# Kernel tuning notes

Measured on AMD Instinct MI355X. Metric: run time of the kernel, lower is better.

## Reference

```python
import jax, jax.numpy as jnp
import numpy as np

B, IN, U = 16, 1024, 1024


def _wSw(W, S):
    # W: [i,u], S: [b,i,i] -> W^T S W : [b,u,u]
    return jnp.einsum('iu,bij,jv->buv', W, S, W)


def _xSx(x, Wsig):
    # (sum_i x_i^2) * W_Sigma, broadcast over batch
    return jnp.sum(x * x, axis=1)[:, None, None] * Wsig


def _trS(S, Wsig):
    return jnp.trace(S, axis1=1, axis2=2)[:, None, None] * Wsig


def _hadamard_sigma(s1, s2, m1, m2):
    # s1*s2 + diag(m1) s2 diag(m1) + diag(m2) s1 diag(m2)
    return (s1 * s2
            + m1[:, :, None] * s2 * m1[:, None, :]
            + m2[:, :, None] * s1 * m2[:, None, :])


def _act_sigma(g, S):
    # S * outer(g, g)
    return S * (g[:, :, None] * g[:, None, :])


def setup_inputs() -> dict:
    key = jax.random.key(0)
    ks = jax.random.split(key, 16)
    f32 = jnp.float32
    init_mu, ini_sigma = 0.05, -4.6
    inp = {
        'mu_inputs': jax.random.normal(ks[0], (B, IN), f32),
        'sigma_inputs': 0.01 * jax.random.normal(ks[1], (B, IN, IN), f32),
        'prev_state': 0.1 * jax.random.normal(ks[2], (B, U), f32),
        'Sigma_state': 0.01 * jax.random.normal(ks[3], (B, U, U), f32),
        'U_z': init_mu * jax.random.normal(ks[4], (IN, U), f32),
        'uz_sigma': jnp.full((U,), ini_sigma, f32),
        'W_z': init_mu * jax.random.normal(ks[5], (U, U), f32),
        'wz_sigma': jnp.full((U,), ini_sigma, f32),
        'U_r': init_mu * jax.random.normal(ks[6], (IN, U), f32),
        'ur_sigma': jnp.full((U,), ini_sigma, f32),
        'W_r': init_mu * jax.random.normal(ks[7], (U, U), f32),
        'wr_sigma': jnp.full((U,), ini_sigma, f32),
        'U_h': init_mu * jax.random.normal(ks[8], (IN, U), f32),
        'uh_sigma': jnp.full((U,), ini_sigma, f32),
        'W_h': init_mu * jax.random.normal(ks[9], (U, U), f32),
        'wh_sigma': jnp.full((U,), ini_sigma, f32),
    }
    return inp


def reference(mu_inputs, sigma_inputs, prev_state, Sigma_state,
              U_z, uz_sigma, W_z, wz_sigma,
              U_r, ur_sigma, W_r, wr_sigma,
              U_h, uh_sigma, W_h, wh_sigma):
    sp = jax.nn.softplus
    # ---- z gate ----
    pre_z = mu_inputs @ U_z + prev_state @ W_z
    z = jax.nn.sigmoid(pre_z)
    Uz_S, Wz_S = jnp.diag(sp(uz_sigma)), jnp.diag(sp(wz_sigma))
    Sigma_zz = (_wSw(U_z, sigma_inputs) + _xSx(mu_inputs, Uz_S) + _trS(sigma_inputs, Uz_S)
                + _wSw(W_z, Sigma_state) + _xSx(prev_state, Wz_S) + _trS(Sigma_state, Wz_S))
    Sigma_z = _act_sigma(z * (1.0 - z), Sigma_zz)  # analytic d sigmoid
    # ---- r gate ----
    pre_r = mu_inputs @ U_r + prev_state @ W_r
    r = jax.nn.sigmoid(pre_r)
    Ur_S, Wr_S = jnp.diag(sp(ur_sigma)), jnp.diag(sp(wr_sigma))
    Sigma_rr = (_wSw(U_r, sigma_inputs) + _xSx(mu_inputs, Ur_S) + _trS(sigma_inputs, Ur_S)
                + _wSw(W_r, Sigma_state) + _xSx(prev_state, Wr_S) + _trS(Sigma_state, Wr_S))
    Sigma_r = _act_sigma(r * (1.0 - r), Sigma_rr)
    # ---- h gate ----
    sr = prev_state * r
    pre_h = mu_inputs @ U_h + sr @ W_h
    h = jnp.tanh(pre_h)
    Uh_S, Wh_S = jnp.diag(sp(uh_sigma)), jnp.diag(sp(wh_sigma))
    sigma_g = _hadamard_sigma(Sigma_state, Sigma_r, prev_state, r)
    Sigma_hh = (_wSw(U_h, sigma_inputs) + _xSx(mu_inputs, Uh_S) + _trS(sigma_inputs, Uh_S)
                + _wSw(W_h, sigma_g) + _xSx(sr, Wh_S) + _trS(sigma_g, Wh_S))
    Sigma_h = _act_sigma(1.0 - h * h, Sigma_hh)  # analytic d tanh
    # ---- combine ----
    mu_out = z * prev_state + (1.0 - z) * h
    sigma_a = _hadamard_sigma(Sigma_z, Sigma_state, z, prev_state)
    sigma_b = _hadamard_sigma(Sigma_z, Sigma_h, 1.0 - z, h)
    sigma_ab = Sigma_z * (prev_state[:, :, None] * h[:, None, :])
    sigma_abT = Sigma_z * (h[:, :, None] * prev_state[:, None, :])
    Sigma_out = sigma_a + sigma_b - sigma_ab - sigma_abT
    Sigma_out = jnp.where(jnp.isfinite(Sigma_out), Sigma_out, jnp.zeros_like(Sigma_out))
    eye = jnp.eye(Sigma_out.shape[-1], dtype=bool)
    Sigma_out = jnp.where(eye, jnp.abs(Sigma_out), Sigma_out)
    return mu_out, Sigma_out
```

## Files before the change

kernel.cpp:

```cpp
#include <hip/hip_runtime.h>
#include <math.h>


#define B_  16
#define N_  1024
#define NN_ (1024*1024)

typedef __bf16 bf16x8 __attribute__((ext_vector_type(8)));
typedef float  f32x4  __attribute__((ext_vector_type(4)));
typedef unsigned short ushort8v __attribute__((ext_vector_type(8)));

__device__ __forceinline__ unsigned short f2bf(float f) {
  union { float f; unsigned int u; } v; v.f = f;
  unsigned int r = v.u + 0x7fffu + ((v.u >> 16) & 1u);
  return (unsigned short)(r >> 16);
}
__device__ __forceinline__ float bf2f(unsigned short h) {
  union { unsigned int u; float f; } v; v.u = ((unsigned int)h) << 16;
  return v.f;
}

__device__ __forceinline__ void gload_lds16(const void* g, void* l) {
  __builtin_amdgcn_global_load_lds((__attribute__((address_space(1))) void*)g,
                                   (__attribute__((address_space(3))) void*)l,
                                   16, 0, 0);
}

#define MFMA_ __builtin_amdgcn_mfma_f32_16x16x32_bf16
#define SYNC_()  do { asm volatile("s_waitcnt lgkmcnt(0)" ::: "memory"); \
                      __builtin_amdgcn_sched_barrier(0); \
                      __builtin_amdgcn_s_barrier(); \
                      __builtin_amdgcn_sched_barrier(0); } while (0)

template<int OMODE, int PAIR>
__global__ __launch_bounds__(512)
void gemm8p(const unsigned short* __restrict__ A, int lda, long aStride, int koffA,
            const unsigned short* __restrict__ Bm, const unsigned short* __restrict__ Bm2,
            int ldb, long bStride, int K,
            void* __restrict__ Out, int ldo, long oStride, int noff,
            const float* __restrict__ act,
            const float* __restrict__ spU, const float* __restrict__ spW,
            const float* __restrict__ dU, const float* __restrict__ dW,
            const unsigned short* __restrict__ SzP, const float* __restrict__ SstP,
            const float* __restrict__ zV, const float* __restrict__ prevV,
            const float* __restrict__ hV)
{
  __shared__ __align__(16) char ldsb[163840];
  const int id = blockIdx.x;
  const int xcd = id & 7, rest = id >> 3;
  const int mt = rest & 3, pp = rest >> 2;
  const int panel = xcd + (pp << 3);
  const int nt = panel & 3;
  const int b  = (panel >> 2) & 15;
  const int ps = PAIR ? (panel >> 6) : 0;
  const unsigned short* Bsel = (PAIR && ps) ? Bm2 : Bm;
  const int kofx = koffA + (ps ? 1024 : 0);
  const int nofx = noff  + (ps ? 1024 : 0);
  const int mbase = mt << 8, nbase = nt << 8;
  const int tid = threadIdx.x, lane = tid & 63, w = tid >> 6;
  const int wm = w >> 2, wn = w & 3;
  const int NT = K >> 6;

  f32x4 acc[8][4];
  const f32x4 zero4 = {0.f, 0.f, 0.f, 0.f};
#pragma unroll
  for (int i = 0; i < 8; i++)
#pragma unroll
    for (int j = 0; j < 4; j++) acc[i][j] = zero4;

  const int l3 = lane >> 3, l7 = lane & 7;
  const int posg = l7 ^ l3;
  const int gr = (l3 << 1) + (posg >> 2);
  const int gc = (posg & 3) << 3;
  const int bi0 = w << 1, bi1 = bi0 + 1;
  const int rS0 = ((bi0 >> 1) << 4) + gr, cS0 = ((bi0 & 1) << 5) + gc;
  const int rS1 = ((bi1 >> 1) << 4) + gr, cS1 = ((bi1 & 1) << 5) + gc;
  const unsigned short* Ab = A + (size_t)b * aStride + (size_t)mbase * lda + kofx;
  const unsigned short* Bb = Bsel + (size_t)b * bStride + (size_t)nbase * ldb;
  const int d0 = w << 11, d1 = (w << 11) + 1024;

  auto SA = [&](int tt, int h) {
    char* dst = ldsb + ((tt & 1) << 15) + (h << 14);
    const unsigned short* s = Ab + (size_t)(h << 7) * lda + ((size_t)tt << 6);
    gload_lds16(s + (size_t)rS0 * lda + cS0, dst + d0);
    gload_lds16(s + (size_t)rS1 * lda + cS1, dst + d1);
  };
  auto SB = [&](int tt, int h) {
    char* dst = ldsb + 65536 + (tt % 3) * 32768 + (h << 14);
    const unsigned short* s = Bb + (size_t)(h << 7) * ldb + ((size_t)tt << 6);
    gload_lds16(s + (size_t)rS0 * ldb + cS0, dst + d0);
    gload_lds16(s + (size_t)rS1 * ldb + cS1, dst + d1);
  };

  const int lrow = lane & 15, c4 = lane >> 4;
  const int aoff = ((lrow >> 1) << 7) + (((((lrow & 1) << 2) | c4) ^ (lrow >> 1)) << 4);
  const int abase = wm << 14;
  const int bbase = ((wn >> 1) << 14);
  const int brg   = (wn & 1) << 2;
  auto LDA = [&](const char* pa, int mi, int ks) -> bf16x8 {
    return *(const bf16x8*)(pa + abase + (((mi << 1) + ks) << 10) + aoff);
  };
  auto LDB = [&](const char* pbv, int ni, int ks) -> bf16x8 {
    return *(const bf16x8*)(pbv + bbase + ((((brg + ni) << 1) + ks) << 10) + aoff);
  };

  SA(0, 0); SA(0, 1); SB(0, 0); SB(0, 1);
  if (NT > 1) { SB(1, 0); SB(1, 1); }
  asm volatile("s_waitcnt vmcnt(4)" ::: "memory");
  __builtin_amdgcn_sched_barrier(0);
  __builtin_amdgcn_s_barrier();
  __builtin_amdgcn_sched_barrier(0);

  bf16x8 avA[4], avB[4], bvA[4], bvB[4];
#pragma unroll
  for (int i = 0; i < 4; i++) avB[i] = LDA(ldsb, i, 0);
#pragma unroll
  for (int i = 0; i < 4; i++) bvB[i] = LDB(ldsb + 65536, i, 0);
  __builtin_amdgcn_sched_barrier(0);

  int bs = 0;
  for (int kt = 0; kt < NT; ++kt) {
    const char* pa = ldsb + ((kt & 1) << 15);
    const char* pbv = ldsb + 65536 + bs * 32768;
    const int bsn = (bs == 2) ? 0 : bs + 1;
    const char* pan = ldsb + (((kt + 1) & 1) << 15);
    const char* pbn = ldsb + 65536 + bsn * 32768;
#pragma unroll
    for (int i = 0; i < 4; i++) avA[i] = LDA(pa, 4 + i, 0);
    if (kt + 1 < NT) SA(kt + 1, 0);
    __builtin_amdgcn_s_setprio(1);
#pragma unroll
    for (int ni = 0; ni < 4; ni++)
#pragma unroll
      for (int mi = 0; mi < 4; mi++)
        acc[mi][ni] = MFMA_(avB[mi], bvB[ni], acc[mi][ni], 0, 0, 0);
    __builtin_amdgcn_s_setprio(0);
#pragma unroll
    for (int i = 0; i < 4; i++) avB[i] = LDA(pa, i, 1);
#pragma unroll
    for (int i = 0; i < 4; i++) bvA[i] = LDB(pbv, i, 1);
    if (kt + 1 < NT) SA(kt + 1, 1);
    __builtin_amdgcn_s_setprio(1);
#pragma unroll
    for (int ni = 0; ni < 4; ni++)
#pragma unroll
      for (int mi = 0; mi < 4; mi++)
        acc[4 + mi][ni] = MFMA_(avA[mi], bvB[ni], acc[4 + mi][ni], 0, 0, 0);
    __builtin_amdgcn_s_setprio(0);
#pragma unroll
    for (int i = 0; i < 4; i++) avA[i] = LDA(pa, 4 + i, 1);
    __builtin_amdgcn_s_setprio(1);
#pragma unroll
    for (int ni = 0; ni < 4; ni++)
#pragma unroll
      for (int mi = 0; mi < 4; mi++)
        acc[mi][ni] = MFMA_(avB[mi], bvA[ni], acc[mi][ni], 0, 0, 0);
    __builtin_amdgcn_s_setprio(0);
    if (kt + 2 < NT) {
      SB(kt + 2, 0); SB(kt + 2, 1);
      asm volatile("s_waitcnt vmcnt(4)" ::: "memory");
    } else {
      asm volatile("s_waitcnt vmcnt(0)" ::: "memory");
    }
    SYNC_();
    if (kt + 1 < NT) {
#pragma unroll
      for (int i = 0; i < 4; i++) avB[i] = LDA(pan, i, 0);
#pragma unroll
      for (int i = 0; i < 4; i++) bvB[i] = LDB(pbn, i, 0);
    }
    __builtin_amdgcn_sched_barrier(0);
    __builtin_amdgcn_s_setprio(1);
#pragma unroll
    for (int ni = 0; ni < 4; ni++)
#pragma unroll
      for (int mi = 0; mi < 4; mi++)
        acc[4 + mi][ni] = MFMA_(avA[mi], bvA[ni], acc[4 + mi][ni], 0, 0, 0);
    __builtin_amdgcn_s_setprio(0);
    bs = bsn;
  }

  __syncthreads();
  unsigned short* scr = (unsigned short*)(ldsb + w * 16384);
  const float* actb = act ? (act + b * N_) : nullptr;
  float dUb = 0.f, dWb = 0.f;
  if (OMODE != 0) { dUb = dU[b]; dWb = dW[b]; }

#pragma unroll
  for (int mi = 0; mi < 8; mi++) {
    const int rl0 = mi * 16 + ((lane >> 4) << 2);
#pragma unroll
    for (int ni = 0; ni < 4; ni++) {
      const int cl = ni * 16 + (lane & 15);
#pragma unroll
      for (int r = 0; r < 4; r++) {
        const int rl = rl0 + r;
        float val = acc[mi][ni][r];
        if (OMODE != 0) {
          const int u = mbase + wm * 128 + rl, v = nbase + wn * 64 + cl;
          if (u == v) val += dUb * spU[u] + dWb * spW[u];
          val *= actb[u] * actb[v];
        }
        scr[rl * 64 + ((((cl >> 3) ^ (rl & 7))) << 3) + (cl & 7)] = f2bf(val);
      }
    }
  }
  asm volatile("s_waitcnt lgkmcnt(0)" ::: "memory");
  __builtin_amdgcn_sched_barrier(0);

#pragma unroll
  for (int pq = 0; pq < 16; pq++) {
    const int row = pq * 8 + (lane >> 3);
    const int slot = lane & 7;
    const int ch = slot ^ (row & 7);
    const int u = mbase + wm * 128 + row;
    const int v0 = nbase + wn * 64 + (ch << 3);
    ushort8v s8 = *(const ushort8v*)&scr[row * 64 + (slot << 3)];
    if (OMODE == 0 || OMODE == 1) {
      unsigned short* ob = (unsigned short*)Out + (size_t)b * oStride
                         + (size_t)u * ldo + nofx + v0;
      *(ushort8v*)ob = s8;
    } else if (OMODE == 3) {
      const float pu = prevV[b * N_ + u];
      const float ru = zV[b * N_ + u];
      const ushort8v st8 = *(const ushort8v*)(SzP + (size_t)b * NN_ + (size_t)u * N_ + v0);
      const f32x4 pv0 = *(const f32x4*)(prevV + b * N_ + v0);
      const f32x4 pv1 = *(const f32x4*)(prevV + b * N_ + v0 + 4);
      const f32x4 rv0 = *(const f32x4*)(zV + b * N_ + v0);
      const f32x4 rv1 = *(const f32x4*)(zV + b * N_ + v0 + 4);
      ushort8v o8;
#pragma unroll
      for (int q = 0; q < 8; q++) {
        const float srv = bf2f((unsigned short)s8[q]);
        const float stt = bf2f((unsigned short)st8[q]);
        const float pv = (q < 4) ? pv0[q] : pv1[q - 4];
        const float rv = (q < 4) ? rv0[q] : rv1[q - 4];
        o8[q] = f2bf(stt * srv + pu * pv * srv + ru * rv * stt);
      }
      unsigned short* ob = (unsigned short*)Out + (size_t)b * oStride
                         + (size_t)u * ldo + v0;
      *(ushort8v*)ob = o8;
    } else {
      const float zu = zV[b * N_ + u];
      const float pu = prevV[b * N_ + u];
      const float hu = hV[b * N_ + u];
      const ushort8v sz8 = *(const ushort8v*)(SzP + (size_t)b * NN_ + (size_t)u * N_ + v0);
      const f32x4 st0 = *(const f32x4*)(SstP + (size_t)b * NN_ + (size_t)u * N_ + v0);
      const f32x4 st1 = *(const f32x4*)(SstP + (size_t)b * NN_ + (size_t)u * N_ + v0 + 4);
      const f32x4 zv0 = *(const f32x4*)(zV + b * N_ + v0);
      const f32x4 zv1 = *(const f32x4*)(zV + b * N_ + v0 + 4);
      const f32x4 pv0 = *(const f32x4*)(prevV + b * N_ + v0);
      const f32x4 pv1 = *(const f32x4*)(prevV + b * N_ + v0 + 4);
      const f32x4 hv0 = *(const f32x4*)(hV + b * N_ + v0);
      const f32x4 hv1 = *(const f32x4*)(hV + b * N_ + v0 + 4);
      f32x4 o0, o1;
#pragma unroll
      for (int q = 0; q < 8; q++) {
        const float shh = bf2f((unsigned short)s8[q]);
        const float szv = bf2f((unsigned short)sz8[q]);
        const float stt = (q < 4) ? st0[q] : st1[q - 4];
        const float zv  = (q < 4) ? zv0[q] : zv1[q - 4];
        const float pv  = (q < 4) ? pv0[q] : pv1[q - 4];
        const float hv  = (q < 4) ? hv0[q] : hv1[q - 4];
        float res = szv * stt + zu * zv * stt + pu * pv * szv
                  + szv * shh + (1.f - zu) * (1.f - zv) * shh + hu * hv * szv
                  - szv * (pu * hv) - szv * (hu * pv);
        if (!isfinite(res)) res = 0.f;
        if (u == v0 + q) res = fabsf(res);
        if (q < 4) o0[q] = res; else o1[q - 4] = res;
      }
      float* ob = (float*)Out + (size_t)b * oStride + (size_t)u * ldo + v0;
      *(f32x4*)ob = o0;
      *(f32x4*)(ob + 4) = o1;
    }
  }
}


__global__ void conv_bf16_2(const float* __restrict__ in0, unsigned short* __restrict__ out0,
                            const float* __restrict__ in1, unsigned short* __restrict__ out1,
                            int n4)
{
  const float* in = blockIdx.y ? in1 : in0;
  unsigned short* out = blockIdx.y ? out1 : out0;
  int i = blockIdx.x * 256 + threadIdx.x;
  const int stride = gridDim.x * 256;
  for (; i < n4; i += stride) {
    const float4 v = ((const float4*)in)[i];
    ushort4 o;
    o.x = f2bf(v.x); o.y = f2bf(v.y); o.z = f2bf(v.z); o.w = f2bf(v.w);
    ((ushort4*)out)[i] = o;
  }
}

__global__ void build_AT(const float* __restrict__ Uz, const float* __restrict__ Wz,
                         const float* __restrict__ Ur, const float* __restrict__ Wr,
                         const float* __restrict__ Uh, const float* __restrict__ Wh,
                         unsigned short* __restrict__ AT)
{
  __shared__ float tile[32][33];
  const int g = blockIdx.z;
  const float* U = g == 0 ? Uz : (g == 1 ? Ur : Uh);
  const float* W = g == 0 ? Wz : (g == 1 ? Wr : Wh);
  const int u0  = blockIdx.x * 32;
  const int k0g = blockIdx.y * 32;
  const float* src = (k0g >= 1024) ? W : U;
  const int kloc = k0g & 1023;
  const int tx = threadIdx.x & 31, ty = threadIdx.x >> 5;
  unsigned short* out = AT + (size_t)g * N_ * 2048;
#pragma unroll
  for (int i = 0; i < 32; i += 8) tile[ty + i][tx] = src[(size_t)(kloc + ty + i) * N_ + u0 + tx];
  __syncthreads();
#pragma unroll
  for (int i = 0; i < 32; i += 8)
    out[(size_t)(u0 + ty + i) * 2048 + k0g + tx] = f2bf(tile[tx][ty + i]);
}

__global__ void softplus6(const float* a0, const float* a1, const float* a2,
                          const float* a3, const float* a4, const float* a5,
                          float* __restrict__ sp)
{
  const float* src[6] = {a0, a1, a2, a3, a4, a5};
  const int g = blockIdx.x;
  const float* s = src[g];
  for (int i = threadIdx.x; i < N_; i += 256) {
    float x = s[i];
    sp[g * N_ + i] = (x > 20.f) ? x : log1pf(expf(x));
  }
}

__global__ void scalars1(const float* __restrict__ mu, const float* __restrict__ prev,
                         const float* __restrict__ sin_, const float* __restrict__ Sst,
                         float* __restrict__ dA, float* __restrict__ dBzr)
{
  __shared__ float red[256];
  const int b = blockIdx.x;
  float s1 = 0.f, s2 = 0.f;
  for (int i = threadIdx.x; i < N_; i += 256) {
    const float m = mu[b * N_ + i];
    s1 += m * m + sin_[(size_t)b * NN_ + (size_t)i * (N_ + 1)];
    const float p = prev[b * N_ + i];
    s2 += p * p + Sst[(size_t)b * NN_ + (size_t)i * (N_ + 1)];
  }
  red[threadIdx.x] = s1; __syncthreads();
  for (int s = 128; s > 0; s >>= 1) { if (threadIdx.x < s) red[threadIdx.x] += red[threadIdx.x + s]; __syncthreads(); }
  if (threadIdx.x == 0) dA[b] = red[0];
  __syncthreads();
  red[threadIdx.x] = s2; __syncthreads();
  for (int s = 128; s > 0; s >>= 1) { if (threadIdx.x < s) red[threadIdx.x] += red[threadIdx.x + s]; __syncthreads(); }
  if (threadIdx.x == 0) dBzr[b] = red[0];
}

__global__ __launch_bounds__(256)
void gate_pre2(const float* __restrict__ x1, const float* __restrict__ x2,
               const float* __restrict__ U0, const float* __restrict__ W0,
               const float* __restrict__ U1, const float* __restrict__ W1,
               float* __restrict__ Ppart)
{
  const int g  = blockIdx.z;
  const int ks = blockIdx.y;
  const int out = blockIdx.x * 256 + threadIdx.x;
  const int b = out >> 10, col = out & 1023;
  const float* x = (ks < 4) ? x1 : x2;
  const float* Wm = (g == 0) ? ((ks < 4) ? U0 : W0) : ((ks < 4) ? U1 : W1);
  const int k0 = (ks & 3) * 256;
  const float* xb = x + b * N_ + k0;
  const float* wp = Wm + (size_t)k0 * N_ + col;
  float acc = 0.f;
#pragma unroll 8
  for (int k = 0; k < 256; k++)
    acc += xb[k] * wp[(size_t)k * N_];
  Ppart[(g * 8 + ks) * (B_ * N_) + out] = acc;
}

__global__ void gate_act2(const float* __restrict__ P,
                          float* __restrict__ z, float* __restrict__ gz,
                          float* __restrict__ r, float* __restrict__ gr)
{
  const int out = blockIdx.x * 256 + threadIdx.x;
  float a0 = 0.f, a1 = 0.f;
#pragma unroll
  for (int ks = 0; ks < 8; ks++) {
    a0 += P[ks * (B_ * N_) + out];
    a1 += P[(8 + ks) * (B_ * N_) + out];
  }
  const float s0 = 1.f / (1.f + expf(-a0));
  const float s1 = 1.f / (1.f + expf(-a1));
  z[out] = s0; gz[out] = s0 * (1.f - s0);
  r[out] = s1; gr[out] = s1 * (1.f - s1);
}

__global__ __launch_bounds__(256)
void gate_pre1(const float* __restrict__ x1, const float* __restrict__ x2,
               const float* __restrict__ U0, const float* __restrict__ W0,
               float* __restrict__ Ppart)
{
  const int ks = blockIdx.y;
  const int out = blockIdx.x * 256 + threadIdx.x;
  const int b = out >> 10, col = out & 1023;
  const float* x = (ks < 4) ? x1 : x2;
  const float* Wm = (ks < 4) ? U0 : W0;
  const int k0 = (ks & 3) * 256;
  const float* xb = x + b * N_ + k0;
  const float* wp = Wm + (size_t)k0 * N_ + col;
  float acc = 0.f;
#pragma unroll 8
  for (int k = 0; k < 256; k++)
    acc += xb[k] * wp[(size_t)k * N_];
  Ppart[ks * (B_ * N_) + out] = acc;
}

__global__ void gate_act1(const float* __restrict__ P,
                          const float* __restrict__ z, const float* __restrict__ prev,
                          float* __restrict__ h, float* __restrict__ gh,
                          float* __restrict__ mu_out)
{
  const int out = blockIdx.x * 256 + threadIdx.x;
  float a0 = 0.f;
#pragma unroll
  for (int ks = 0; ks < 8; ks++) a0 += P[ks * (B_ * N_) + out];
  const float s = tanhf(a0);
  h[out] = s; gh[out] = 1.f - s * s;
  const float zz = z[out];
  mu_out[out] = zz * prev[out] + (1.f - zz) * s;
}

__global__ void sr_csr(const float* __restrict__ prev, const float* __restrict__ r,
                       float* __restrict__ sr, float* __restrict__ csr)
{
  __shared__ float red[256];
  const int b = blockIdx.x;
  float s = 0.f;
  for (int i = threadIdx.x; i < N_; i += 256) {
    const float v = prev[b * N_ + i] * r[b * N_ + i];
    sr[b * N_ + i] = v;
    s += v * v;
  }
  red[threadIdx.x] = s; __syncthreads();
  for (int k = 128; k > 0; k >>= 1) { if (threadIdx.x < k) red[threadIdx.x] += red[threadIdx.x + k]; __syncthreads(); }
  if (threadIdx.x == 0) csr[b] = red[0];
}

__global__ void scalars2(const unsigned short* __restrict__ Sg,
                         const float* __restrict__ csr, float* __restrict__ dBh)
{
  __shared__ float red[256];
  const int b = blockIdx.x;
  float s = 0.f;
  for (int i = threadIdx.x; i < N_; i += 256)
    s += bf2f(Sg[(size_t)b * NN_ + (size_t)i * (N_ + 1)]);
  red[threadIdx.x] = s; __syncthreads();
  for (int k = 128; k > 0; k >>= 1) { if (threadIdx.x < k) red[threadIdx.x] += red[threadIdx.x + k]; __syncthreads(); }
  if (threadIdx.x == 0) dBh[b] = red[0] + csr[b];
}


extern "C" void kernel_launch(void* const* d_in, const int* in_sizes, int n_in,
                              void* d_out, int out_size, void* d_ws, size_t ws_size,
                              hipStream_t stream)
{
  const float* mu   = (const float*)d_in[0];
  const float* sin_ = (const float*)d_in[1];
  const float* prev = (const float*)d_in[2];
  const float* Sst  = (const float*)d_in[3];
  const float* Uz = (const float*)d_in[4];  const float* uzs = (const float*)d_in[5];
  const float* Wz = (const float*)d_in[6];  const float* wzs = (const float*)d_in[7];
  const float* Ur = (const float*)d_in[8];  const float* urs = (const float*)d_in[9];
  const float* Wr = (const float*)d_in[10]; const float* wrs = (const float*)d_in[11];
  const float* Uh = (const float*)d_in[12]; const float* uhs = (const float*)d_in[13];
  const float* Wh = (const float*)d_in[14]; const float* whs = (const float*)d_in[15];

  char* ws = (char*)d_ws;
  size_t off = 0;
  auto take = [&](size_t bytes) -> char* {
    char* p = ws + off;
    off = (off + bytes + 255) & ~(size_t)255;
    return p;
  };
  unsigned short* Tcm = (unsigned short*)take((size_t)B_ * 2048 * 1024 * 2);
  unsigned short* Sz  = (unsigned short*)take((size_t)B_ * NN_ * 2);
  unsigned short* Sg  = (unsigned short*)take((size_t)B_ * NN_ * 2);
  unsigned short* AT  = (unsigned short*)take((size_t)3 * N_ * 2048 * 2);
  float* Ppart = (float*)take((size_t)16 * B_ * N_ * 4);
  float* sp   = (float*)take(6 * N_ * 4);
  float* z    = (float*)take(B_ * N_ * 4);
  float* gz   = (float*)take(B_ * N_ * 4);
  float* rr   = (float*)take(B_ * N_ * 4);
  float* gr   = (float*)take(B_ * N_ * 4);
  float* h    = (float*)take(B_ * N_ * 4);
  float* gh   = (float*)take(B_ * N_ * 4);
  float* sr   = (float*)take(B_ * N_ * 4);
  float* dA   = (float*)take(64);
  float* dBzr = (float*)take(64);
  float* dBh  = (float*)take(64);
  float* csr  = (float*)take(64);
  if (off > ws_size) return;

  float* mu_out = (float*)d_out;
  float* SigOut = (float*)d_out + (size_t)B_ * N_;
  unsigned short* SinH = (unsigned short*)SigOut;
  unsigned short* SstH = (unsigned short*)SigOut + (size_t)B_ * NN_;

  const unsigned short* ATz = AT;
  const unsigned short* ATr = AT + (size_t)N_ * 2048;
  const unsigned short* ATh = AT + (size_t)2 * N_ * 2048;

  conv_bf16_2<<<dim3(2048, 2), 256, 0, stream>>>(sin_, SinH, Sst, SstH, B_ * NN_ / 4);
  softplus6<<<6, 256, 0, stream>>>(uzs, wzs, urs, wrs, uhs, whs, sp);
  scalars1<<<16, 256, 0, stream>>>(mu, prev, sin_, Sst, dA, dBzr);
  build_AT<<<dim3(32, 64, 3), 256, 0, stream>>>(Uz, Wz, Ur, Wr, Uh, Wh, AT);
  gate_pre2<<<dim3(64, 8, 2), 256, 0, stream>>>(mu, prev, Uz, Wz, Ur, Wr, Ppart);
  gate_act2<<<64, 256, 0, stream>>>(Ppart, z, gz, rr, gr);
  sr_csr<<<16, 256, 0, stream>>>(prev, rr, sr, csr);
  gate_pre1<<<dim3(64, 8), 256, 0, stream>>>(mu, sr, Uh, Wh, Ppart);
  gate_act1<<<64, 256, 0, stream>>>(Ppart, z, prev, h, gh, mu_out);

  const long tS = (long)2048 * 1024;

  gemm8p<0, 1><<<512, 512, 0, stream>>>(ATz, 2048, 0, 0, SinH, SstH, 1024, (long)NN_, 1024,
                                        Tcm, 2048, tS, 0, nullptr, nullptr, nullptr, nullptr, nullptr,
                                        nullptr, nullptr, nullptr, nullptr, nullptr);
  gemm8p<1, 0><<<256, 512, 0, stream>>>(ATz, 2048, 0, 0, Tcm, nullptr, 2048, tS, 2048,
                                        Sz, 1024, (long)NN_, 0, gz, sp + 0, sp + 1024, dA, dBzr,
                                        nullptr, nullptr, nullptr, nullptr, nullptr);
  gemm8p<0, 1><<<512, 512, 0, stream>>>(ATr, 2048, 0, 0, SinH, SstH, 1024, (long)NN_, 1024,
                                        Tcm, 2048, tS, 0, nullptr, nullptr, nullptr, nullptr, nullptr,
                                        nullptr, nullptr, nullptr, nullptr, nullptr);
  gemm8p<3, 0><<<256, 512, 0, stream>>>(ATr, 2048, 0, 0, Tcm, nullptr, 2048, tS, 2048,
                                        Sg, 1024, (long)NN_, 0, gr, sp + 2048, sp + 3072, dA, dBzr,
                                        SstH, nullptr, rr, prev, nullptr);
  scalars2<<<16, 256, 0, stream>>>(Sg, csr, dBh);
  gemm8p<0, 1><<<512, 512, 0, stream>>>(ATh, 2048, 0, 0, SinH, Sg, 1024, (long)NN_, 1024,
                                        Tcm, 2048, tS, 0, nullptr, nullptr, nullptr, nullptr, nullptr,
                                        nullptr, nullptr, nullptr, nullptr, nullptr);
  gemm8p<2, 0><<<256, 512, 0, stream>>>(ATh, 2048, 0, 0, Tcm, nullptr, 2048, tS, 2048,
                                        SigOut, 1024, (long)NN_, 0, gh, sp + 4096, sp + 5120, dA, dBh,
                                        Sz, Sst, z, prev, h);
}
```

Measured before the change: 514.6 us.

## Load A operand fragments directly from global memory instead of staging through LDS

The GEMM kernel no longer stages the A tile through LDS. Each lane now reads its bf16x8 MFMA fragments straight from global memory, and LDS shrinks to hold only the triple-buffered B tiles. This removes the LDS traffic and footprint for A and could allow higher occupancy. In exchange, each wave issues uncoalesced-ish global loads on the critical path with no explicit prefetch, and rows shared between waves are fetched redundantly. It also adds an empty no-op loop in scalars2.

Result: slower. 952.8 us (+85.2%).

```diff
diff --git a/kernel.cpp b/kernel.cpp
--- a/kernel.cpp
+++ b/kernel.cpp
@@ -45,7 +45,7 @@
             const float* __restrict__ zV, const float* __restrict__ prevV,
             const float* __restrict__ hV)
 {
-  __shared__ __align__(16) char ldsb[163840];
+  __shared__ __align__(16) char ldsb[131072];
   const int id = blockIdx.x;
   const int xcd = id & 7, rest = id >> 3;
   const int mt = rest & 3, pp = rest >> 2;
@@ -75,36 +75,30 @@
   const int bi0 = w << 1, bi1 = bi0 + 1;
   const int rS0 = ((bi0 >> 1) << 4) + gr, cS0 = ((bi0 & 1) << 5) + gc;
   const int rS1 = ((bi1 >> 1) << 4) + gr, cS1 = ((bi1 & 1) << 5) + gc;
-  const unsigned short* Ab = A + (size_t)b * aStride + (size_t)mbase * lda + kofx;
   const unsigned short* Bb = Bsel + (size_t)b * bStride + (size_t)nbase * ldb;
   const int d0 = w << 11, d1 = (w << 11) + 1024;
 
-  auto SA = [&](int tt, int h) {
-    char* dst = ldsb + ((tt & 1) << 15) + (h << 14);
-    const unsigned short* s = Ab + (size_t)(h << 7) * lda + ((size_t)tt << 6);
-    gload_lds16(s + (size_t)rS0 * lda + cS0, dst + d0);
-    gload_lds16(s + (size_t)rS1 * lda + cS1, dst + d1);
-  };
   auto SB = [&](int tt, int h) {
-    char* dst = ldsb + 65536 + (tt % 3) * 32768 + (h << 14);
+    char* dst = ldsb + (tt % 3) * 32768 + (h << 14);
     const unsigned short* s = Bb + (size_t)(h << 7) * ldb + ((size_t)tt << 6);
     gload_lds16(s + (size_t)rS0 * ldb + cS0, dst + d0);
     gload_lds16(s + (size_t)rS1 * ldb + cS1, dst + d1);
   };
 
   const int lrow = lane & 15, c4 = lane >> 4;
+  const unsigned short* Alane = A + (size_t)b * aStride
+      + (size_t)(mbase + wm * 128 + lrow) * lda + kofx + (c4 << 3);
+  auto AG = [&](int tt, int mf, int ks) -> bf16x8 {
+    return *(const bf16x8*)(Alane + (size_t)(mf << 4) * lda + ((size_t)tt << 6) + (ks << 5));
+  };
   const int aoff = ((lrow >> 1) << 7) + (((((lrow & 1) << 2) | c4) ^ (lrow >> 1)) << 4);
-  const int abase = wm << 14;
   const int bbase = ((wn >> 1) << 14);
   const int brg   = (wn & 1) << 2;
-  auto LDA = [&](const char* pa, int mi, int ks) -> bf16x8 {
-    return *(const bf16x8*)(pa + abase + (((mi << 1) + ks) << 10) + aoff);
-  };
   auto LDB = [&](const char* pbv, int ni, int ks) -> bf16x8 {
     return *(const bf16x8*)(pbv + bbase + ((((brg + ni) << 1) + ks) << 10) + aoff);
   };
 
-  SA(0, 0); SA(0, 1); SB(0, 0); SB(0, 1);
+  SB(0, 0); SB(0, 1);
   if (NT > 1) { SB(1, 0); SB(1, 1); }
   asm volatile("s_waitcnt vmcnt(4)" ::: "memory");
   __builtin_amdgcn_sched_barrier(0);
@@ -113,21 +107,18 @@
 
   bf16x8 avA[4], avB[4], bvA[4], bvB[4];
 #pragma unroll
-  for (int i = 0; i < 4; i++) avB[i] = LDA(ldsb, i, 0);
-#pragma unroll
-  for (int i = 0; i < 4; i++) bvB[i] = LDB(ldsb + 65536, i, 0);
+  for (int i = 0; i < 4; i++) avB[i] = AG(0, i, 0);
+#pragma unroll
+  for (int i = 0; i < 4; i++) bvB[i] = LDB(ldsb, i, 0);
   __builtin_amdgcn_sched_barrier(0);
 
   int bs = 0;
   for (int kt = 0; kt < NT; ++kt) {
-    const char* pa = ldsb + ((kt & 1) << 15);
-    const char* pbv = ldsb + 65536 + bs * 32768;
+    const char* pbv = ldsb + bs * 32768;
     const int bsn = (bs == 2) ? 0 : bs + 1;
-    const char* pan = ldsb + (((kt + 1) & 1) << 15);
-    const char* pbn = ldsb + 65536 + bsn * 32768;
-#pragma unroll
-    for (int i = 0; i < 4; i++) avA[i] = LDA(pa, 4 + i, 0);
-    if (kt + 1 < NT) SA(kt + 1, 0);
+    const char* pbn = ldsb + bsn * 32768;
+#pragma unroll
+    for (int i = 0; i < 4; i++) avA[i] = AG(kt, 4 + i, 0);
     __builtin_amdgcn_s_setprio(1);
 #pragma unroll
     for (int ni = 0; ni < 4; ni++)
@@ -136,10 +127,9 @@
         acc[mi][ni] = MFMA_(avB[mi], bvB[ni], acc[mi][ni], 0, 0, 0);
     __builtin_amdgcn_s_setprio(0);
 #pragma unroll
-    for (int i = 0; i < 4; i++) avB[i] = LDA(pa, i, 1);
+    for (int i = 0; i < 4; i++) avB[i] = AG(kt, i, 1);
 #pragma unroll
     for (int i = 0; i < 4; i++) bvA[i] = LDB(pbv, i, 1);
-    if (kt + 1 < NT) SA(kt + 1, 1);
     __builtin_amdgcn_s_setprio(1);
 #pragma unroll
     for (int ni = 0; ni < 4; ni++)
@@ -148,7 +138,7 @@
         acc[4 + mi][ni] = MFMA_(avA[mi], bvB[ni], acc[4 + mi][ni], 0, 0, 0);
     __builtin_amdgcn_s_setprio(0);
 #pragma unroll
-    for (int i = 0; i < 4; i++) avA[i] = LDA(pa, 4 + i, 1);
+    for (int i = 0; i < 4; i++) avA[i] = AG(kt, 4 + i, 1);
     __builtin_amdgcn_s_setprio(1);
 #pragma unroll
     for (int ni = 0; ni < 4; ni++)
@@ -165,7 +155,7 @@
     SYNC_();
     if (kt + 1 < NT) {
 #pragma unroll
-      for (int i = 0; i < 4; i++) avB[i] = LDA(pan, i, 0);
+      for (int i = 0; i < 4; i++) avB[i] = AG(kt + 1, i, 0);
 #pragma unroll
       for (int i = 0; i < 4; i++) bvB[i] = LDB(pbn, i, 0);
     }
@@ -447,6 +437,9 @@
   __shared__ float red[256];
   const int b = blockIdx.x;
   float s = 0.f;
+  for (int i = threadIdx.x; i < 256 * 4; i += 256)
+    ;
+  s = 0.f;
   for (int i = threadIdx.x; i < N_; i += 256)
     s += bf2f(Sg[(size_t)b * NN_ + (size_t)i * (N_ + 1)]);
   red[threadIdx.x] = s; __syncthreads();
```
